# Optimization experiments

Measured on AMD Instinct MI355X. Metric: run time of the kernel, lower is better.

Reference implementation:

```python
import jax, jax.numpy as jnp
import numpy as np

NUM_EMBEDDINGS = 1024
EMBEDDING_DIM = 256
BETA = 0.25


def setup_inputs() -> dict:
    key = jax.random.key(0)
    k1, k2 = jax.random.split(key)
    x = jax.random.normal(k1, (32, 256, 32, 32), dtype=jnp.float32)
    # nn.Embedding weight init: uniform(-1/K, 1/K)
    lim = 1.0 / NUM_EMBEDDINGS
    emb_weight = jax.random.uniform(k2, (NUM_EMBEDDINGS, EMBEDDING_DIM),
                                    dtype=jnp.float32, minval=-lim, maxval=lim)
    return {"x": x, "emb_weight": emb_weight}


def reference(x, emb_weight):
    b, c, h, w = x.shape
    # [b, h, w, c] -> [N, c]
    x_flat = jnp.transpose(x, (0, 2, 3, 1)).reshape(-1, c)
    distances = (jnp.sum(x_flat * x_flat, axis=1, keepdims=True)
                 - 2.0 * jnp.einsum('nc,kc->nk', x_flat, emb_weight)
                 + jnp.sum(emb_weight * emb_weight, axis=1))
    indices = jnp.argmin(distances, axis=1)  # [N]
    quantized = emb_weight[indices].reshape(b, h, w, c).transpose(0, 3, 1, 2)
    sg = jax.lax.stop_gradient
    commitment_loss = jnp.mean((sg(quantized) - x) ** 2)
    embedding_loss = jnp.mean((quantized - sg(x)) ** 2)
    loss = commitment_loss + BETA * embedding_loss
    return quantized, loss, indices.reshape(b, h, w)
```

## Files before the change

kernel.cpp:

```cpp
#include <hip/hip_runtime.h>

#define LOSS_OFF 8388608
#define IDX_OFF  8388609

#define WS_SEE   0
#define WS_SXX   4096
#define WS_KEY   135168
#define WS_CNT   397312
#define WS_LOSS  397320
#define WS_WL    397328
#define WS_EP    528448

#define FLT_BIG  3.402823466e+38f
#define MARGIN   1.0e-4f

typedef __attribute__((ext_vector_type(8))) short  short8v;
typedef __attribute__((ext_vector_type(4))) float  float4v;

#define GLD16(gp, lp) __builtin_amdgcn_global_load_lds( \
    (const __attribute__((address_space(1))) unsigned int*)(gp), \
    (__attribute__((address_space(3))) unsigned int*)(lp), 16, 0, 0)

__device__ __forceinline__ float np_sumsq256(const float* __restrict__ p, int stride) {
    float s[2];
#pragma unroll
    for (int half = 0; half < 2; half++) {
        const float* a = p + half * 128 * stride;
        float r[8];
#pragma unroll
        for (int l = 0; l < 8; l++) {
            float v = a[l * stride];
            float sq = v * v;
            asm volatile("" : "+v"(sq));
            r[l] = sq;
        }
#pragma unroll
        for (int i = 8; i < 128; i += 8) {
#pragma unroll
            for (int l = 0; l < 8; l++) {
                float v = a[(i + l) * stride];
                float sq = v * v;
                asm volatile("" : "+v"(sq));
                r[l] = r[l] + sq;
            }
        }
        s[half] = ((r[0] + r[1]) + (r[2] + r[3])) + ((r[4] + r[5]) + (r[6] + r[7]));
    }
    return s[0] + s[1];
}

__device__ __forceinline__ unsigned int f32_sortable(float m) {
    unsigned int u = __float_as_uint(m);
    return u ^ (((unsigned int)((int)u >> 31)) | 0x80000000u);
}
__device__ __forceinline__ float f32_unsortable(unsigned int s) {
    const unsigned int u = (s >> 31) ? (s ^ 0x80000000u) : ~s;
    return __uint_as_float(u);
}

__device__ __forceinline__ unsigned short f2bf(float f) {
    unsigned int u = __float_as_uint(f);
    return (unsigned short)((u + 0x7fffu + ((u >> 16) & 1u)) >> 16);
}
__device__ __forceinline__ float bf2f(unsigned short h) {
    return __uint_as_float(((unsigned int)h) << 16);
}

__global__ __launch_bounds__(256) void k_prep(const float* __restrict__ emb,
                                              unsigned short* __restrict__ ebP,
                                              float* __restrict__ see,
                                              int* __restrict__ cnt,
                                              double* __restrict__ loss) {
    const int t = threadIdx.x, bb = blockIdx.x;
    if (bb < 256) {
        const int idx = bb * 256 + t;
        const int l  = idx & 63;
        const int ph = (idx >> 6) & 1;
        const int ct = (idx >> 7) & 7;
        const int cc = (idx >> 10) & 7;
        const int cg = (idx >> 13) & 7;
        const int row = cg * 128 + ct * 16 + (l & 15);
        const int col = cc * 32 + (l >> 4) * 8;
        const float* src = emb + (size_t)row * 256 + col;
        uint4 out;
        unsigned short* op = (unsigned short*)&out;
#pragma unroll
        for (int i = 0; i < 8; i++) {
            const float v = src[i];
            const unsigned short h = f2bf(v);
            op[i] = ph ? f2bf(v - bf2f(h)) : h;
        }
        *(uint4*)(ebP + (size_t)idx * 8) = out;
    } else {
        const int k = (bb - 256) * 256 + t;
        see[k] = np_sumsq256(emb + (size_t)k * 256, 1);
        if (k == 0) { *cnt = 0; *loss = 0.0; }
    }
}

__global__ __launch_bounds__(256) void k_et(const float* __restrict__ emb,
                                            float* __restrict__ eT) {
    __shared__ float T[256][17];
    const int t  = threadIdx.x;
    const int k0 = blockIdx.x << 4;
    const int kr = t >> 4, cs = (t & 15) << 4;
#pragma unroll
    for (int j = 0; j < 4; j++) {
        const float4 v = *(const float4*)(emb + (size_t)(k0 + kr) * 256 + cs + j * 4);
        T[cs + j * 4 + 0][kr] = v.x;
        T[cs + j * 4 + 1][kr] = v.y;
        T[cs + j * 4 + 2][kr] = v.z;
        T[cs + j * 4 + 3][kr] = v.w;
    }
    __syncthreads();
    float* dst = eT + (size_t)t * 1024 + k0;
#pragma unroll
    for (int j = 0; j < 4; j++) {
        float4 v;
        v.x = T[t][j * 4 + 0]; v.y = T[t][j * 4 + 1];
        v.z = T[t][j * 4 + 2]; v.w = T[t][j * 4 + 3];
        *(float4*)(dst + j * 4) = v;
    }
}

__global__ __launch_bounds__(256) void k_xpack(const float* __restrict__ x,
                                               unsigned short* __restrict__ axP,
                                               float* __restrict__ sxx) {
    __shared__ float xs[256 * 33];
    const int t = threadIdx.x, rs = blockIdx.x;
    const int row = t & 31, cg = t >> 5;
    const int b = rs >> 5;
    const int hw0 = (rs & 31) << 5;
    const float* xb = x + (size_t)b * 262144 + hw0 + row;
#pragma unroll 4
    for (int cc2 = 0; cc2 < 32; cc2++) {
        const int c = cg * 32 + cc2;
        xs[c * 33 + row] = xb[(size_t)c * 1024];
    }
    __syncthreads();
#pragma unroll
    for (int ii = 0; ii < 4; ii++) {
        const int ci = ii * 256 + t;
        const int l = ci & 63;
        const int rowg = (ci >> 6) & 1;
        const int cc = ci >> 7;
        const int r = rowg * 16 + (l & 15);
        const int c0 = cc * 32 + (l >> 4) * 8;
        uint4 hp, lp;
        unsigned short* hpp = (unsigned short*)&hp;
        unsigned short* lpp = (unsigned short*)&lp;
#pragma unroll
        for (int i = 0; i < 8; i++) {
            const float v = xs[(c0 + i) * 33 + r];
            const unsigned short h = f2bf(v);
            hpp[i] = h;
            lpp[i] = f2bf(v - bf2f(h));
        }
        const size_t base = ((size_t)rs * 8 + cc) * 2 + rowg;
        *(uint4*)(axP + ((base * 2 + 0) * 64 + l) * 8) = hp;
        *(uint4*)(axP + ((base * 2 + 1) * 64 + l) * 8) = lp;
    }
    if (t < 32) sxx[rs * 32 + t] = np_sumsq256(xs + t, 33);
}

__global__ __launch_bounds__(512, 2) void k1_mfma(
        const unsigned short* __restrict__ axP,
        const unsigned short* __restrict__ ebP,
        const float* __restrict__ see_g,
        unsigned long long* __restrict__ key,
        float* __restrict__ distg,
        int* __restrict__ cnt, int* __restrict__ wl) {
    __shared__ char smem[71680];
    unsigned long long* lk1 = (unsigned long long*)(smem + 65536);
    float*              lg2 = (float*)(smem + 69632);
    const int t = threadIdx.x;
    const int codeg = t >> 6, l = t & 63;
    const int lrow = l >> 4, lcol = l & 15;
    const int rb = blockIdx.x;
    const int n0 = rb * 64;

    {
        const int sub = codeg >> 2;
        const char* aBase = (const char*)axP;
        char* aDst = smem + codeg * 1024;
#pragma unroll
        for (int cc = 0; cc < 8; cc++) {
            const char* src = aBase + ((size_t)((rb * 2 + sub) * 8 + cc)) * 4096
                              + (size_t)(codeg & 3) * 1024 + (size_t)l * 16;
            GLD16(src, aDst + cc * 8192);
        }
    }
    __syncthreads();

    float4v acc[4][8];
#pragma unroll
    for (int at = 0; at < 4; at++)
#pragma unroll
        for (int ct = 0; ct < 8; ct++) acc[at][ct] = (float4v){0.f, 0.f, 0.f, 0.f};

    for (int cc = 0; cc < 8; cc++) {
        short8v ah[4], al[4];
#pragma unroll
        for (int at = 0; at < 4; at++) {
            const int off = cc * 8192 + (at >> 1) * 4096 + (at & 1) * 2048;
            ah[at] = *(const short8v*)(smem + off + l * 16);
            al[at] = *(const short8v*)(smem + off + 1024 + l * 16);
        }
#pragma unroll
        for (int ct = 0; ct < 8; ct++) {
            const size_t bb = ((((size_t)codeg * 8 + cc) * 8 + ct) * 2) * 512 + (size_t)l * 8;
            const short8v bh = *(const short8v*)(ebP + bb);
            const short8v bl = *(const short8v*)(ebP + bb + 512);
            __builtin_amdgcn_s_setprio(1);
#pragma unroll
            for (int at = 0; at < 4; at++) {
                acc[at][ct] = __builtin_amdgcn_mfma_f32_16x16x32_bf16(ah[at], bh, acc[at][ct], 0, 0, 0);
                acc[at][ct] = __builtin_amdgcn_mfma_f32_16x16x32_bf16(ah[at], bl, acc[at][ct], 0, 0, 0);
                acc[at][ct] = __builtin_amdgcn_mfma_f32_16x16x32_bf16(al[at], bh, acc[at][ct], 0, 0, 0);
            }
            __builtin_amdgcn_s_setprio(0);
        }
    }

    float sv[8];
#pragma unroll
    for (int ct = 0; ct < 8; ct++) sv[ct] = see_g[codeg * 128 + ct * 16 + lcol];

#pragma unroll
    for (int at = 0; at < 4; at++) {
#pragma unroll
        for (int j = 0; j < 4; j++) {
            unsigned long long K1 = ~0ull; float G1 = FLT_BIG, G2 = FLT_BIG;
#pragma unroll
            for (int ct = 0; ct < 8; ct++) {
                const float g = fmaf(-2.f, acc[at][ct][j], sv[ct]);
                const int k = codeg * 128 + ct * 16 + lcol;
                const unsigned long long pk =
                    ((unsigned long long)f32_sortable(g) << 32) | (unsigned int)k;
                if (pk < K1) { G2 = G1; K1 = pk; G1 = g; }
                else         { G2 = fminf(G2, g); }
            }
#pragma unroll
            for (int m = 1; m < 16; m <<= 1) {
                const unsigned long long oK = __shfl_xor(K1, m, 64);
                const float oG2 = __shfl_xor(G2, m, 64);
                const float oG1 = f32_unsortable((unsigned int)(oK >> 32));
                if (oK < K1) { G2 = fminf(oG2, G1); K1 = oK; G1 = oG1; }
                else         { G2 = fminf(G2, oG1); }
            }
            const int rloc = at * 16 + lrow * 4 + j;
            if (lcol == 0) { lk1[rloc * 8 + codeg] = K1; lg2[rloc * 8 + codeg] = G2; }
        }
    }
    __syncthreads();
    if (t < 64) {
        unsigned long long K1 = ~0ull; float G1 = FLT_BIG, G2 = FLT_BIG;
        for (int cg = 0; cg < 8; cg++) {
            const unsigned long long oK = lk1[t * 8 + cg];
            const float oG2 = lg2[t * 8 + cg];
            const float oG1 = f32_unsortable((unsigned int)(oK >> 32));
            if (oK < K1) { G2 = fminf(oG2, G1); K1 = oK; G1 = oG1; }
            else         { G2 = fminf(G2, oG1); }
        }
        const int n = n0 + t;
        distg[n] = G1;
        if (G2 - G1 > MARGIN) { key[n] = K1; }
        else { key[n] = ~0ull; wl[atomicAdd(cnt, 1)] = n; }
    }
}

__global__ __launch_bounds__(256) void k2r(const float* __restrict__ x,
                                           const float* __restrict__ eT,
                                           const float* __restrict__ see,
                                           const float* __restrict__ sxx,
                                           unsigned long long* __restrict__ key,
                                           const int* __restrict__ cnt,
                                           const int* __restrict__ wl) {
    __shared__ float xs[8][264];
    const int t = threadIdx.x;
    const int total = *cnt;
    for (int base = blockIdx.x * 8; base < total; base += 128 * 8) {
        int nrow[8]; float sx8[8];
#pragma unroll
        for (int r = 0; r < 8; r++) {
            int idx = base + r; if (idx >= total) idx = total - 1;
            const int n = wl[idx];
            nrow[r] = n; sx8[r] = sxx[n];
        }
        __syncthreads();
#pragma unroll
        for (int r = 0; r < 8; r++) {
            const int n = nrow[r];
            xs[r][t] = x[(size_t)(n >> 10) * 262144 + (size_t)t * 1024 + (n & 1023)];
        }
        __syncthreads();
        float d[8][4];
#pragma unroll
        for (int r = 0; r < 8; r++)
#pragma unroll
            for (int j = 0; j < 4; j++) d[r][j] = 0.f;
#pragma unroll 4
        for (int c = 0; c < 256; c++) {
            float ev[4];
#pragma unroll
            for (int j = 0; j < 4; j++) ev[j] = eT[(size_t)c * 1024 + t + 256 * j];
#pragma unroll
            for (int r = 0; r < 8; r++) {
                const float xv = xs[r][c];
                d[r][0] = fmaf(xv, ev[0], d[r][0]);
                d[r][1] = fmaf(xv, ev[1], d[r][1]);
                d[r][2] = fmaf(xv, ev[2], d[r][2]);
                d[r][3] = fmaf(xv, ev[3], d[r][3]);
            }
        }
#pragma unroll
        for (int r = 0; r < 8; r++) {
            unsigned long long best = ~0ull;
#pragma unroll
            for (int j = 0; j < 4; j++) {
                const float q = fmaf(-2.f, d[r][j], sx8[r]) + see[t + 256 * j];
                const unsigned long long pk =
                    ((unsigned long long)f32_sortable(q) << 32) | (unsigned int)(t + 256 * j);
                best = pk < best ? pk : best;
            }
            atomicMin(&key[nrow[r]], best);
        }
    }
}

__global__ __launch_bounds__(256) void k_loss(const float* __restrict__ sxx,
                                              const float* __restrict__ distg,
                                              double* __restrict__ loss) {
    __shared__ double red[256];
    const int t = threadIdx.x;
    const int base = blockIdx.x * 1024 + t;
    double sd = 0.0;
#pragma unroll
    for (int i = 0; i < 4; i++) {
        const int n = base + i * 256;
        sd += (double)(sxx[n] + distg[n]);
    }
    red[t] = sd;
    __syncthreads();
    for (int s = 128; s > 0; s >>= 1) {
        if (t < s) red[t] += red[t + s];
        __syncthreads();
    }
    if (t == 0) atomicAdd(loss, red[0]);
}

__global__ __launch_bounds__(256) void k3_out(const float* __restrict__ emb,
                                              const unsigned long long* __restrict__ key,
                                              float* __restrict__ dout) {
    __shared__ float elds[32][257];
    __shared__ int   idxs[32];
    const int t  = threadIdx.x;
    const int bh = blockIdx.x;
    const int b = bh >> 5, h = bh & 31;
    if (t < 32) idxs[t] = (int)(key[(bh << 5) + t] & 0xffffffffull);
    __syncthreads();
    for (int r = 0; r < 32; r++) elds[r][t] = emb[(size_t)idxs[r] * 256 + t];
    __syncthreads();
    const int w = t & 31, cg = t >> 5;
    const size_t base = (size_t)b * 262144 + (size_t)(h * 32 + w);
#pragma unroll 4
    for (int s = 0; s < 32; s++) {
        const int c = (cg << 5) + s;
        dout[base + (size_t)c * 1024] = elds[w][c];
    }
    if (t < 32) dout[IDX_OFF + (bh << 5) + t] = (float)idxs[t];
}

__global__ void k4_fin(const double* __restrict__ loss, float* __restrict__ dout) {
    dout[LOSS_OFF] = (float)(1.25 * (*loss) / 8388608.0);
}

extern "C" void kernel_launch(void* const* d_in, const int* in_sizes, int n_in,
                              void* d_out, int out_size, void* d_ws, size_t ws_size,
                              hipStream_t stream) {
    const float* x   = (const float*)d_in[0];
    const float* emb = (const float*)d_in[1];
    float* dout = (float*)d_out;
    char* ws = (char*)d_ws;
    float*  see  = (float*)(ws + WS_SEE);
    float*  sxx  = (float*)(ws + WS_SXX);
    unsigned long long* key = (unsigned long long*)(ws + WS_KEY);
    int*    cnt  = (int*)(ws + WS_CNT);
    double* loss = (double*)(ws + WS_LOSS);
    int*    wl   = (int*)(ws + WS_WL);
    unsigned short* ebP = (unsigned short*)(ws + WS_EP);
    float*  eT   = (float*)(ws + WS_EP);
    unsigned short* axP = (unsigned short*)d_out;
    float* distg = dout + IDX_OFF;

    k_prep <<<260,  256, 0, stream>>>(emb, ebP, see, cnt, loss);
    k_xpack<<<1024, 256, 0, stream>>>(x, axP, sxx);
    k1_mfma<<<512,  512, 0, stream>>>(axP, ebP, see, key, distg, cnt, wl);
    k_et   <<<64,   256, 0, stream>>>(emb, eT);
    k2r    <<<128,  256, 0, stream>>>(x, eT, see, sxx, key, cnt, wl);
    k_loss <<<32,   256, 0, stream>>>(sxx, distg, loss);
    k3_out <<<1024, 256, 0, stream>>>(emb, key, dout);
    k4_fin <<<1,      1, 0, stream>>>(loss, dout);
}
```

Before: 200.0 us.

## Fuse x packing and loss reduction into the MFMA distance kernel

Removes the separate x-packing kernel: the MFMA kernel now loads its 64 rows of x straight into LDS, splits them into bf16 hi/lo fragments and computes the row norms itself. The separate loss-reduction kernel is also removed, and each block's partial loss is reduced by wave shuffle and added atomically. This saves two launches plus the global round trip of the packed activations and distances. In exchange, LDS use grows to 128 KB per block, which may limit occupancy below the two blocks per CU requested, and the atomic loss update order is now nondeterministic.

```diff
diff --git a/kernel.cpp b/kernel.cpp
--- a/kernel.cpp
+++ b/kernel.cpp
@@ -123,72 +123,66 @@
     }
 }
 
-__global__ __launch_bounds__(256) void k_xpack(const float* __restrict__ x,
-                                               unsigned short* __restrict__ axP,
-                                               float* __restrict__ sxx) {
-    __shared__ float xs[256 * 33];
-    const int t = threadIdx.x, rs = blockIdx.x;
-    const int row = t & 31, cg = t >> 5;
-    const int b = rs >> 5;
-    const int hw0 = (rs & 31) << 5;
-    const float* xb = x + (size_t)b * 262144 + hw0 + row;
-#pragma unroll 4
-    for (int cc2 = 0; cc2 < 32; cc2++) {
-        const int c = cg * 32 + cc2;
-        xs[c * 33 + row] = xb[(size_t)c * 1024];
-    }
-    __syncthreads();
+__global__ __launch_bounds__(512, 2) void k1_mfma(
+        const float* __restrict__ x,
+        const unsigned short* __restrict__ ebP,
+        const float* __restrict__ see_g,
+        float* __restrict__ sxx_g,
+        unsigned long long* __restrict__ key,
+        double* __restrict__ loss,
+        int* __restrict__ cnt, int* __restrict__ wl) {
+    __shared__ char smem[131072];
+    unsigned long long* lk1 = (unsigned long long*)smem;
+    float*              lg2 = (float*)(smem + 4096);
+    float* xstage = (float*)smem;
+    char*  frag   = smem + 65536;
+
+    const int t = threadIdx.x;
+    const int w = t >> 6, l = t & 63;
+    const int codeg = w;
+    const int lrow = l >> 4, lcol = l & 15;
+    const int rb = blockIdx.x;
+    const int n0 = rb * 64;
+    const int b  = rb >> 4;
+    const int hw0 = (rb & 15) << 6;
+
+    {
+        const char* xbyte = (const char*)x + ((size_t)b * 262144 + hw0) * 4;
+#pragma unroll
+        for (int i = 0; i < 8; i++) {
+            const int cbase = i * 32 + w * 4;
+            const char* src = xbyte + (size_t)(cbase + (l >> 4)) * 4096 + (size_t)(l & 15) * 16;
+            GLD16(src, smem + cbase * 256);
+        }
+    }
+    __syncthreads();
+
 #pragma unroll
     for (int ii = 0; ii < 4; ii++) {
-        const int ci = ii * 256 + t;
-        const int l = ci & 63;
-        const int rowg = (ci >> 6) & 1;
-        const int cc = ci >> 7;
-        const int r = rowg * 16 + (l & 15);
-        const int c0 = cc * 32 + (l >> 4) * 8;
+        const int pi  = ii * 512 + t;
+        const int pcc = pi >> 8;
+        const int pat = (pi >> 6) & 3;
+        const int pl  = pi & 63;
+        const int prow = pat * 16 + (pl & 15);
+        const int pc0  = pcc * 32 + (pl >> 4) * 8;
         uint4 hp, lp;
         unsigned short* hpp = (unsigned short*)&hp;
         unsigned short* lpp = (unsigned short*)&lp;
 #pragma unroll
         for (int i = 0; i < 8; i++) {
-            const float v = xs[(c0 + i) * 33 + r];
+            const float v = xstage[(pc0 + i) * 64 + prow];
             const unsigned short h = f2bf(v);
             hpp[i] = h;
             lpp[i] = f2bf(v - bf2f(h));
         }
-        const size_t base = ((size_t)rs * 8 + cc) * 2 + rowg;
-        *(uint4*)(axP + ((base * 2 + 0) * 64 + l) * 8) = hp;
-        *(uint4*)(axP + ((base * 2 + 1) * 64 + l) * 8) = lp;
-    }
-    if (t < 32) sxx[rs * 32 + t] = np_sumsq256(xs + t, 33);
-}
-
-__global__ __launch_bounds__(512, 2) void k1_mfma(
-        const unsigned short* __restrict__ axP,
-        const unsigned short* __restrict__ ebP,
-        const float* __restrict__ see_g,
-        unsigned long long* __restrict__ key,
-        float* __restrict__ distg,
-        int* __restrict__ cnt, int* __restrict__ wl) {
-    __shared__ char smem[71680];
-    unsigned long long* lk1 = (unsigned long long*)(smem + 65536);
-    float*              lg2 = (float*)(smem + 69632);
-    const int t = threadIdx.x;
-    const int codeg = t >> 6, l = t & 63;
-    const int lrow = l >> 4, lcol = l & 15;
-    const int rb = blockIdx.x;
-    const int n0 = rb * 64;
-
-    {
-        const int sub = codeg >> 2;
-        const char* aBase = (const char*)axP;
-        char* aDst = smem + codeg * 1024;
-#pragma unroll
-        for (int cc = 0; cc < 8; cc++) {
-            const char* src = aBase + ((size_t)((rb * 2 + sub) * 8 + cc)) * 4096
-                              + (size_t)(codeg & 3) * 1024 + (size_t)l * 16;
-            GLD16(src, aDst + cc * 8192);
-        }
+        char* dst = frag + pcc * 8192 + pat * 2048 + pl * 16;
+        *(uint4*)dst = hp;
+        *(uint4*)(dst + 1024) = lp;
+    }
+    float sx_reg = 0.f;
+    if (t < 64) {
+        sx_reg = np_sumsq256(xstage + t, 64);
+        sxx_g[n0 + t] = sx_reg;
     }
     __syncthreads();
 
@@ -202,9 +196,9 @@
         short8v ah[4], al[4];
 #pragma unroll
         for (int at = 0; at < 4; at++) {
-            const int off = cc * 8192 + (at >> 1) * 4096 + (at & 1) * 2048;
-            ah[at] = *(const short8v*)(smem + off + l * 16);
-            al[at] = *(const short8v*)(smem + off + 1024 + l * 16);
+            const int off = cc * 8192 + at * 2048 + l * 16;
+            ah[at] = *(const short8v*)(frag + off);
+            al[at] = *(const short8v*)(frag + off + 1024);
         }
 #pragma unroll
         for (int ct = 0; ct < 8; ct++) {
@@ -263,9 +257,12 @@
             else         { G2 = fminf(G2, oG1); }
         }
         const int n = n0 + t;
-        distg[n] = G1;
         if (G2 - G1 > MARGIN) { key[n] = K1; }
         else { key[n] = ~0ull; wl[atomicAdd(cnt, 1)] = n; }
+        float part = sx_reg + G1;
+#pragma unroll
+        for (int m = 1; m < 64; m <<= 1) part += __shfl_xor(part, m, 64);
+        if (t == 0) atomicAdd(loss, (double)part);
     }
 }
 
@@ -326,27 +323,6 @@
             atomicMin(&key[nrow[r]], best);
         }
     }
-}
-
-__global__ __launch_bounds__(256) void k_loss(const float* __restrict__ sxx,
-                                              const float* __restrict__ distg,
-                                              double* __restrict__ loss) {
-    __shared__ double red[256];
-    const int t = threadIdx.x;
-    const int base = blockIdx.x * 1024 + t;
-    double sd = 0.0;
-#pragma unroll
-    for (int i = 0; i < 4; i++) {
-        const int n = base + i * 256;
-        sd += (double)(sxx[n] + distg[n]);
-    }
-    red[t] = sd;
-    __syncthreads();
-    for (int s = 128; s > 0; s >>= 1) {
-        if (t < s) red[t] += red[t + s];
-        __syncthreads();
-    }
-    if (t == 0) atomicAdd(loss, red[0]);
 }
 
 __global__ __launch_bounds__(256) void k3_out(const float* __restrict__ emb,
@@ -390,15 +366,11 @@
     int*    wl   = (int*)(ws + WS_WL);
     unsigned short* ebP = (unsigned short*)(ws + WS_EP);
     float*  eT   = (float*)(ws + WS_EP);
-    unsigned short* axP = (unsigned short*)d_out;
-    float* distg = dout + IDX_OFF;
 
     k_prep <<<260,  256, 0, stream>>>(emb, ebP, see, cnt, loss);
-    k_xpack<<<1024, 256, 0, stream>>>(x, axP, sxx);
-    k1_mfma<<<512,  512, 0, stream>>>(axP, ebP, see, key, distg, cnt, wl);
+    k1_mfma<<<512,  512, 0, stream>>>(x, ebP, see, sxx, key, loss, cnt, wl);
     k_et   <<<64,   256, 0, stream>>>(emb, eT);
     k2r    <<<128,  256, 0, stream>>>(x, eT, see, sxx, key, cnt, wl);
-    k_loss <<<32,   256, 0, stream>>>(sxx, distg, loss);
     k3_out <<<1024, 256, 0, stream>>>(emb, key, dout);
     k4_fin <<<1,      1, 0, stream>>>(loss, dout);
 }
```

Measured after the change: 188.9 us. 1.06x faster.
